# Performance work log

Hardware: AMD Instinct MI355X
Metric: run time of the kernel (lower is better)

The kernel has to match this reference:

```python
import jax, jax.numpy as jnp
import numpy as np

P, N, NF = 4, 871, 512            # num_meta_paths, node_size (hardcoded 871 in source), node_feature_size
XDIM = 116 * 116                   # x_proj input dim, hardcoded Linear(116*116, nf)
BETA, LAMBDA_WL, GAMMA = 0.1, 0.1, 0.1


def _xavier(k, shape):
    fan_in, fan_out = shape[0], shape[-1]
    bound = np.sqrt(6.0 / (fan_in + fan_out))
    return jax.random.uniform(k, shape, jnp.float32, -bound, bound)


def setup_inputs() -> dict:
    key = jax.random.key(0)
    ks = jax.random.split(key, 12)
    return {
        "z_stack": jax.random.normal(ks[0], (P, N, NF), jnp.float32),
        "x_orig": jax.random.normal(ks[1], (1, 116, 116), jnp.float32),
        "W": _xavier(ks[2], (N, 1)),
        "b": jax.random.uniform(ks[3], (N, 1), jnp.float32),
        "q": _xavier(ks[4], (N, NF)),
        "xp_w": _xavier(ks[5], (XDIM, NF)),
        "xp_b": jnp.zeros((NF,), jnp.float32),
        "w1": _xavier(ks[6], (2 * NF, 512)), "b1": jnp.zeros((512,), jnp.float32),
        "w2": _xavier(ks[7], (512, 256)), "b2": jnp.zeros((256,), jnp.float32),
        "w3": _xavier(ks[8], (256, 1)), "b3": jnp.zeros((1,), jnp.float32),
        "perm": jax.random.permutation(ks[9], N).astype(jnp.int32),
    }


def _mi_mlp(t, w1, b1, w2, b2, w3, b3):
    h = jax.nn.relu(t @ w1 + b1)
    h = jax.nn.relu(h @ w2 + b2)
    return h @ w3 + b3  # [N, 1]


def reference(z_stack, x_orig, W, b, q, xp_w, xp_b, w1, b1, w2, b2, w3, b3, perm):
    # --- vectorized form of the per-node loop:
    # score_p = mean_i( tanh(W_i * z[p,i,:] + b_i) . q_i )
    zt = jnp.tanh(W[None] * z_stack + b[None])            # [P,N,NF]
    scores = jnp.mean(jnp.sum(zt * q[None], axis=-1), axis=-1)  # [P]
    proportions = scores / jnp.sum(scores)
    attn = jax.nn.softmax(proportions)                    # [P] (no isomorphic pairs -> no overwrite)
    # layer_out_p = attn_p * z_p + z_p ; emb = sum_p layer_out_p
    emb = jnp.einsum('p,pnf->nf', 1.0 + attn, z_stack)    # [N,NF]
    # --- estimate_MI(x_orig, emb, mi_estimator_xz)
    x = jnp.broadcast_to(x_orig.reshape(1, -1), (N, XDIM))
    xh = x @ xp_w + xp_b                                  # [N,NF]
    t0 = jnp.concatenate([xh, emb], axis=1)               # [N,2NF]
    t1 = jnp.concatenate([xh, emb[perm]], axis=1)
    mi_lb = jnp.mean(_mi_mlp(t0, w1, b1, w2, b2, w3, b3)) - jnp.log(
        jnp.mean(jnp.exp(_mi_mlp(t1, w1, b1, w2, b2, w3, b3))) + 1e-8)
    I_XZ = jnp.clip(mi_lb, 0.0)
    # y_labels=None -> I_ZY = 0 ; empty isomorphic_pairs -> wl_loss = 0
    total_loss = I_XZ - BETA * 0.0 + LAMBDA_WL * 0.0 + GAMMA * jnp.sum(attn)
    return emb, total_loss
```

## Files before the change

### kernel.cpp

```cpp
#include <hip/hip_runtime.h>
#include <hip/hip_bf16.h>
#include <math.h>

#define NMETA  4
#define NNODE  871
#define NFEAT  512
#define XDIM   (116*116)
#define ZPLANE (NNODE*NFEAT)
#define MT     55

#define NXB    254
#define XROWS  53

#define WS_CNT    12
#define WS_SPART  16
#define WS_C1P    256
#define WS_XHP    2560
#define WS_V      132608
#define WS_W1P    133504
#define WS_W2P    264576

typedef short v8s __attribute__((ext_vector_type(8)));
typedef float v4f __attribute__((ext_vector_type(4)));

static __device__ __forceinline__ short f2bf(float f) {
  __hip_bfloat16 h = __float2bfloat16(f);
  return *reinterpret_cast<short*>(&h);
}

__global__ __launch_bounds__(1024) void k_front(const float* __restrict__ x,
                                                const float* __restrict__ xpw,
                                                const float* __restrict__ w1,
                                                const float* __restrict__ w2,
                                                const float* __restrict__ z,
                                                const float* __restrict__ W,
                                                const float* __restrict__ b,
                                                const float* __restrict__ q,
                                                float* __restrict__ ws,
                                                short* __restrict__ w1p,
                                                short* __restrict__ w2p) {
  const int blk = blockIdx.x;
  const int tid = threadIdx.x;

  if (blk < NXB) {
    const int d0 = blk * XROWS;
    const int rows = min(XROWS, XDIM - d0);
    __shared__ float xs[XROWS];
    __shared__ float4 redx[7][128];
    if (tid < rows) xs[tid] = x[d0 + tid];
    __syncthreads();
    const int f4 = tid & 127;
    const int g = tid >> 7;
    float4 acc = {0.f, 0.f, 0.f, 0.f};
    const float4* xp4 = (const float4*)xpw;
    for (int r = g; r < rows; r += 8) {
      const float xv = xs[r];
      const float4 wv = xp4[(size_t)(d0 + r) * 128 + f4];
      acc.x += xv * wv.x; acc.y += xv * wv.y; acc.z += xv * wv.z; acc.w += xv * wv.w;
    }
    if (g) redx[g - 1][f4] = acc;
    __syncthreads();
    if (!g) {
#pragma unroll
      for (int k = 0; k < 7; ++k) {
        float4 t = redx[k][f4];
        acc.x += t.x; acc.y += t.y; acc.z += t.z; acc.w += t.w;
      }
      ((float4*)(ws + WS_XHP + (size_t)blk * 512))[f4] = acc;
    }
  } else if (blk < NXB + MT) {
    const int sb = blk - NXB;
    const int row = tid >> 6;
    const int oc = tid & 63;
    const int gr = sb * 16 + row;
    const bool valid = gr < NNODE;
    const float4* z4 = (const float4*)z;
    const float4* q4 = (const float4*)q;
    float4 za0, za1, zb0, zb1, zc0, zc1, zd0, zd1, qa, qb;
    float wi = 0.f, bi = 0.f;
    za0 = za1 = zb0 = zb1 = zc0 = zc1 = zd0 = zd1 = (float4){0,0,0,0};
    qa = qb = (float4){0,0,0,0};
    const int zi = gr * 128 + oc * 2;
    if (valid) {
      za0 = z4[zi];                 za1 = z4[zi + 1];
      zb0 = z4[NNODE*128 + zi];     zb1 = z4[NNODE*128 + zi + 1];
      zc0 = z4[2*NNODE*128 + zi];   zc1 = z4[2*NNODE*128 + zi + 1];
      zd0 = z4[3*NNODE*128 + zi];   zd1 = z4[3*NNODE*128 + zi + 1];
      qa  = q4[zi];                 qb  = q4[zi + 1];
      wi = W[gr]; bi = b[gr];
    }
    auto dot8 = [&](const float4& u0, const float4& u1) -> float {
      return tanhf(wi*u0.x + bi)*qa.x + tanhf(wi*u0.y + bi)*qa.y
           + tanhf(wi*u0.z + bi)*qa.z + tanhf(wi*u0.w + bi)*qa.w
           + tanhf(wi*u1.x + bi)*qb.x + tanhf(wi*u1.y + bi)*qb.y
           + tanhf(wi*u1.z + bi)*qb.z + tanhf(wi*u1.w + bi)*qb.w;
    };
    float sp0 = valid ? dot8(za0, za1) : 0.f;
    float sp1 = valid ? dot8(zb0, zb1) : 0.f;
    float sp2 = valid ? dot8(zc0, zc1) : 0.f;
    float sp3 = valid ? dot8(zd0, zd1) : 0.f;
#pragma unroll
    for (int m = 1; m < 64; m <<= 1) {
      sp0 += __shfl_xor(sp0, m); sp1 += __shfl_xor(sp1, m);
      sp2 += __shfl_xor(sp2, m); sp3 += __shfl_xor(sp3, m);
    }
    __shared__ float sred[16][4];
    if (oc == 0) {
      sred[row][0] = sp0; sred[row][1] = sp1;
      sred[row][2] = sp2; sred[row][3] = sp3;
    }
    __syncthreads();
    if (tid < 4) {
      float s = 0.f;
#pragma unroll
      for (int r = 0; r < 16; ++r) s += sred[r][tid];
      ws[WS_SPART + tid * 55 + sb] = s;
    }
  } else {
    const int pb = blk - (NXB + MT);
    if (pb < 16) {
      const int s0 = pb * 16384;
#pragma unroll
      for (int it = 0; it < 16; ++it) {
        const int s = s0 + it * 1024 + tid;
        const int k = s >> 9, n = s & 511;
        const int t = (k >> 5) * 16384 + (n >> 4) * 512 + ((k >> 3) & 3) * 128
                    + (n & 15) * 8 + (k & 7);
        w1p[t] = f2bf(w1[(size_t)(512 + k) * 512 + n]);
      }
    } else {
      const int o0 = (pb - 16) * 16384;
#pragma unroll
      for (int it = 0; it < 16; ++it) {
        const int o = o0 + it * 1024 + tid;
        const int k = o >> 8, n = o & 255;
        const int t = (k >> 5) * 8192 + (n >> 4) * 512 + ((k >> 3) & 3) * 128
                    + (n & 15) * 8 + (k & 7);
        w2p[t] = f2bf(w2[(size_t)k * 256 + n]);
      }
    }
  }
}

__global__ __launch_bounds__(1024) void k_mid(const float* __restrict__ xpb,
                                              const float* __restrict__ w1,
                                              const float* __restrict__ b1,
                                              float* __restrict__ ws) {
  const int tid = threadIdx.x;
  if (blockIdx.x == 4) {
    if (tid == 0) *(unsigned*)&ws[WS_CNT] = 0u;
    return;
  }
  const int bk = blockIdx.x;
  __shared__ float xh[128];
  __shared__ float redr[1024];
  __shared__ float4 redg[7][128];
  const int f = tid & 127;
  const int part = tid >> 7;
  {
    float s = 0.f;
    for (int p = part; p < NXB; p += 8)
      s += ws[WS_XHP + (size_t)p * 512 + bk * 128 + f];
    redr[tid] = s;
  }
  __syncthreads();
  if (tid < 128) {
    float t = xpb[bk * 128 + tid];
#pragma unroll
    for (int g = 0; g < 8; ++g) t += redr[g * 128 + tid];
    xh[tid] = t;
  }
  __syncthreads();
  const int j4 = tid & 127;
  const int fg = tid >> 7;
  float4 acc = {0.f, 0.f, 0.f, 0.f};
  const float4* w14 = (const float4*)w1;
#pragma unroll
  for (int ff = 0; ff < 16; ++ff) {
    const int fr = bk * 128 + fg * 16 + ff;
    const float xv = xh[fg * 16 + ff];
    const float4 wv = w14[(size_t)fr * 128 + j4];
    acc.x += xv * wv.x; acc.y += xv * wv.y; acc.z += xv * wv.z; acc.w += xv * wv.w;
  }
  if (fg) redg[fg - 1][j4] = acc;
  __syncthreads();
  if (!fg) {
#pragma unroll
    for (int g = 0; g < 7; ++g) {
      float4 t = redg[g][j4];
      acc.x += t.x; acc.y += t.y; acc.z += t.z; acc.w += t.w;
    }
    if (bk == 0) {
      acc.x += b1[j4 * 4 + 0]; acc.y += b1[j4 * 4 + 1];
      acc.z += b1[j4 * 4 + 2]; acc.w += b1[j4 * 4 + 3];
    }
    ((float4*)(ws + WS_C1P + (size_t)bk * 512))[j4] = acc;
  }
}

__global__ __launch_bounds__(1024) void k_fused(const float* __restrict__ z,
                                                float* __restrict__ ws,
                                                float* __restrict__ out,
                                                const short* __restrict__ w1p,
                                                const short* __restrict__ w2p,
                                                const float* __restrict__ b2,
                                                const float* __restrict__ w3,
                                                const float* __restrict__ b3) {
  __shared__ __align__(16) short embs[8192];
  __shared__ __align__(16) short h2a[8192];
  __shared__ float cs[512];
  __shared__ float rf0[1024], rf1[1024];
  __shared__ float vred[16][17];
  __shared__ float cf[4];
  __shared__ float svred[4];
  const int tid = threadIdx.x;
  const int r0 = blockIdx.x * 16;
  const int oc = tid & 63;
  const int row = tid >> 6;
  const int gr = r0 + row;
  const bool valid = gr < NNODE;

  const float4* z4 = (const float4*)z;
  float4 za0, za1, zb0, zb1, zc0, zc1, zd0, zd1;
  za0 = za1 = zb0 = zb1 = zc0 = zc1 = zd0 = zd1 = (float4){0,0,0,0};
  const int zi = gr * 128 + oc * 2;
  if (valid) {
    za0 = z4[zi];                 za1 = z4[zi + 1];
    zb0 = z4[NNODE*128 + zi];     zb1 = z4[NNODE*128 + zi + 1];
    zc0 = z4[2*NNODE*128 + zi];   zc1 = z4[2*NNODE*128 + zi + 1];
    zd0 = z4[3*NNODE*128 + zi];   zd1 = z4[3*NNODE*128 + zi + 1];
  }

  if (tid < 512) {
    float a = 0.f;
#pragma unroll
    for (int k = 0; k < 4; ++k) a += ws[WS_C1P + k * 512 + tid];
    cs[tid] = a;
  }

  {
    const int w4 = tid >> 6;
    if (w4 < 4) {
      float v = (oc < 55) ? ws[WS_SPART + w4 * 55 + oc] : 0.f;
#pragma unroll
      for (int m = 1; m < 64; m <<= 1) v += __shfl_xor(v, m);
      if (oc == 0) svred[w4] = v;
    }
  }
  __syncthreads();
  if (tid == 0) {
    float sv[NMETA], sum = 0.f;
#pragma unroll
    for (int p = 0; p < NMETA; ++p) { sv[p] = svred[p] / (float)NNODE; sum += sv[p]; }
    float m = -1e30f;
#pragma unroll
    for (int p = 0; p < NMETA; ++p) { sv[p] = sv[p] / sum; m = fmaxf(m, sv[p]); }
    float es = 0.f;
#pragma unroll
    for (int p = 0; p < NMETA; ++p) { sv[p] = expf(sv[p] - m); es += sv[p]; }
#pragma unroll
    for (int p = 0; p < NMETA; ++p) cf[p] = 1.f + sv[p] / es;
  }
  __syncthreads();
  const float c0 = cf[0], c1c = cf[1], c2 = cf[2], c3 = cf[3];

  {
    const int slot = oc * 16 + (row ^ (oc & 15));
    v8s h;
    if (valid) {
      float4 r0v, r1v;
      r0v.x = c0*za0.x + c1c*zb0.x + c2*zc0.x + c3*zd0.x;
      r0v.y = c0*za0.y + c1c*zb0.y + c2*zc0.y + c3*zd0.y;
      r0v.z = c0*za0.z + c1c*zb0.z + c2*zc0.z + c3*zd0.z;
      r0v.w = c0*za0.w + c1c*zb0.w + c2*zc0.w + c3*zd0.w;
      r1v.x = c0*za1.x + c1c*zb1.x + c2*zc1.x + c3*zd1.x;
      r1v.y = c0*za1.y + c1c*zb1.y + c2*zc1.y + c3*zd1.y;
      r1v.z = c0*za1.z + c1c*zb1.z + c2*zc1.z + c3*zd1.z;
      r1v.w = c0*za1.w + c1c*zb1.w + c2*zc1.w + c3*zd1.w;
      ((float4*)out)[zi] = r0v;
      ((float4*)out)[zi + 1] = r1v;
      h[0] = f2bf(r0v.x); h[1] = f2bf(r0v.y); h[2] = f2bf(r0v.z); h[3] = f2bf(r0v.w);
      h[4] = f2bf(r1v.x); h[5] = f2bf(r1v.y); h[6] = f2bf(r1v.z); h[7] = f2bf(r1v.w);
    } else {
      h = (v8s){0,0,0,0,0,0,0,0};
    }
    *(v8s*)(embs + slot * 8) = h;
  }
  __syncthreads();

  const int lane = tid & 63, w = tid >> 6;
  const int n15 = lane & 15, quad = lane >> 4;
  v4f e[2];
#pragma unroll
  for (int ct = 0; ct < 2; ++ct) e[ct] = (v4f){0.f, 0.f, 0.f, 0.f};
#pragma unroll
  for (int kb = 0; kb < 16; ++kb) {
    const int koct = kb * 4 + quad;
    v8s a = *(const v8s*)(embs + (koct * 16 + (n15 ^ (koct & 15))) * 8);
    const short* B = w1p + kb * 16384 + w * 1024 + quad * 128 + n15 * 8;
#pragma unroll
    for (int ct = 0; ct < 2; ++ct) {
      v8s bb = *(const v8s*)(B + ct * 512);
      e[ct] = __builtin_amdgcn_mfma_f32_16x16x32_bf16(a, bb, e[ct], 0, 0, 0);
    }
  }
#pragma unroll
  for (int ct = 0; ct < 2; ++ct) {
    const int col = w * 32 + ct * 16 + n15;
    const int koct = col >> 3, j = col & 7;
#pragma unroll
    for (int r = 0; r < 4; ++r) {
      const int m = quad * 4 + r;
      h2a[(koct * 16 + (m ^ (koct & 15))) * 8 + j] = f2bf(fmaxf(e[ct][r] + cs[col], 0.f));
    }
  }
  __syncthreads();

  v4f g = (v4f){0.f, 0.f, 0.f, 0.f};
#pragma unroll
  for (int kb = 0; kb < 16; ++kb) {
    const int koct = kb * 4 + quad;
    v8s a = *(const v8s*)(h2a + (koct * 16 + (n15 ^ (koct & 15))) * 8);
    v8s bb = *(const v8s*)(w2p + kb * 8192 + w * 512 + quad * 128 + n15 * 8);
    g = __builtin_amdgcn_mfma_f32_16x16x32_bf16(a, bb, g, 0, 0, 0);
  }
  {
    const int col = w * 16 + n15;
    const float b2v = b2[col], w3v = w3[col];
#pragma unroll
    for (int r = 0; r < 4; ++r) {
      float s = fmaxf(g[r] + b2v, 0.f) * w3v;
      s += __shfl_xor(s, 1);
      s += __shfl_xor(s, 2);
      s += __shfl_xor(s, 4);
      s += __shfl_xor(s, 8);
      if (n15 == 0) vred[quad * 4 + r][w] = s;
    }
  }
  __syncthreads();
  if (tid < 16) {
    float acc = 0.f;
#pragma unroll
    for (int ww = 0; ww < 16; ++ww) acc += vred[tid][ww];
    const int grow = r0 + tid;
    if (grow < NNODE) ws[WS_V + grow] = acc;
  }

  __shared__ unsigned last;
  __syncthreads();
  if (tid == 0) {
    __threadfence();
    unsigned old = atomicAdd((unsigned int*)&ws[WS_CNT], 1u);
    last = (old == MT - 1) ? 1u : 0u;
  }
  __syncthreads();
  if (last) {
    __builtin_amdgcn_fence(__ATOMIC_ACQUIRE, "agent");
    const float bias = b3[0];
    float s0 = 0.f, s1 = 0.f;
    for (int i = tid; i < NNODE; i += 1024) {
      float xv = ws[WS_V + i] + bias;
      s0 += xv;
      s1 += expf(xv);
    }
    rf0[tid] = s0; rf1[tid] = s1;
    __syncthreads();
    for (int s = 512; s > 0; s >>= 1) {
      if (tid < s) { rf0[tid] += rf0[tid + s]; rf1[tid] += rf1[tid + s]; }
      __syncthreads();
    }
    if (tid == 0) {
      float m0 = rf0[0] / (float)NNODE;
      float m1 = rf1[0] / (float)NNODE;
      float mi = m0 - logf(m1 + 1e-8f);
      out[ZPLANE] = fmaxf(mi, 0.f) + 0.1f;
    }
  }
}

extern "C" void kernel_launch(void* const* d_in, const int* in_sizes, int n_in,
                              void* d_out, int out_size, void* d_ws, size_t ws_size,
                              hipStream_t stream) {
  const float* z   = (const float*)d_in[0];
  const float* x   = (const float*)d_in[1];
  const float* W   = (const float*)d_in[2];
  const float* b   = (const float*)d_in[3];
  const float* q   = (const float*)d_in[4];
  const float* xpw = (const float*)d_in[5];
  const float* xpb = (const float*)d_in[6];
  const float* w1  = (const float*)d_in[7];
  const float* b1  = (const float*)d_in[8];
  const float* w2  = (const float*)d_in[9];
  const float* b2  = (const float*)d_in[10];
  const float* w3  = (const float*)d_in[11];
  const float* b3  = (const float*)d_in[12];
  float* out = (float*)d_out;
  float* ws  = (float*)d_ws;

  short* w1p = (short*)(ws + WS_W1P);
  short* w2p = (short*)(ws + WS_W2P);

  k_front<<<NXB + MT + 20, 1024, 0, stream>>>(x, xpw, w1, w2, z, W, b, q,
                                              ws, w1p, w2p);
  k_mid<<<5, 1024, 0, stream>>>(xpb, w1, b1, ws);
  k_fused<<<MT, 1024, 0, stream>>>(z, ws, out, w1p, w2p, b2, w3, b3);
}
```

Measured before the change: 139.9 us.

## Use output buffer as scratch and replace last-block reduction with atomics plus grid spin barrier

Scratch data (partial sums, packed bf16 weights, counters) now lives inside the output buffer instead of the workspace, and the emb output is written only after all blocks reach a spin barrier, so the scratch regions are overwritten last. The final MI reduction now uses per-block float atomics into two accumulators rather than a last-block pass over per-row values, and k_mid loses its counter-reset block. The grid-wide spin wait assumes all 55 blocks are co-resident, and float atomics make the summation order nondeterministic.

Result: no change. 140.4 us (+0.4%).

```diff
diff --git a/kernel.cpp b/kernel.cpp
--- a/kernel.cpp
+++ b/kernel.cpp
@@ -12,13 +12,14 @@
 #define NXB    254
 #define XROWS  53
 
-#define WS_CNT    12
-#define WS_SPART  16
-#define WS_C1P    256
-#define WS_XHP    2560
-#define WS_V      132608
-#define WS_W1P    133504
-#define WS_W2P    264576
+#define SC_S0     0
+#define SC_S1     1
+#define SC_CNT    2
+#define SC_SPART  16
+#define SC_C1P    256
+#define SC_XHP    2560
+#define SC_W1P    140000
+#define SC_W2P    280000
 
 typedef short v8s __attribute__((ext_vector_type(8)));
 typedef float v4f __attribute__((ext_vector_type(4)));
@@ -36,11 +37,11 @@
                                                 const float* __restrict__ W,
                                                 const float* __restrict__ b,
                                                 const float* __restrict__ q,
-                                                float* __restrict__ ws,
-                                                short* __restrict__ w1p,
-                                                short* __restrict__ w2p) {
+                                                float* __restrict__ out) {
   const int blk = blockIdx.x;
   const int tid = threadIdx.x;
+  short* w1p = (short*)(out + SC_W1P);
+  short* w2p = (short*)(out + SC_W2P);
 
   if (blk < NXB) {
     const int d0 = blk * XROWS;
@@ -66,7 +67,7 @@
         float4 t = redx[k][f4];
         acc.x += t.x; acc.y += t.y; acc.z += t.z; acc.w += t.w;
       }
-      ((float4*)(ws + WS_XHP + (size_t)blk * 512))[f4] = acc;
+      ((float4*)(out + SC_XHP + (size_t)blk * 512))[f4] = acc;
     }
   } else if (blk < NXB + MT) {
     const int sb = blk - NXB;
@@ -114,10 +115,15 @@
       float s = 0.f;
 #pragma unroll
       for (int r = 0; r < 16; ++r) s += sred[r][tid];
-      ws[WS_SPART + tid * 55 + sb] = s;
+      out[SC_SPART + tid * 55 + sb] = s;
     }
   } else {
     const int pb = blk - (NXB + MT);
+    if (pb == 0 && tid == 0) {
+      out[SC_S0] = 0.f;
+      out[SC_S1] = 0.f;
+      *(unsigned*)&out[SC_CNT] = 0u;
+    }
     if (pb < 16) {
       const int s0 = pb * 16384;
 #pragma unroll
@@ -145,12 +151,8 @@
 __global__ __launch_bounds__(1024) void k_mid(const float* __restrict__ xpb,
                                               const float* __restrict__ w1,
                                               const float* __restrict__ b1,
-                                              float* __restrict__ ws) {
+                                              float* __restrict__ out) {
   const int tid = threadIdx.x;
-  if (blockIdx.x == 4) {
-    if (tid == 0) *(unsigned*)&ws[WS_CNT] = 0u;
-    return;
-  }
   const int bk = blockIdx.x;
   __shared__ float xh[128];
   __shared__ float redr[1024];
@@ -160,7 +162,7 @@
   {
     float s = 0.f;
     for (int p = part; p < NXB; p += 8)
-      s += ws[WS_XHP + (size_t)p * 512 + bk * 128 + f];
+      s += out[SC_XHP + (size_t)p * 512 + bk * 128 + f];
     redr[tid] = s;
   }
   __syncthreads();
@@ -194,12 +196,11 @@
       acc.x += b1[j4 * 4 + 0]; acc.y += b1[j4 * 4 + 1];
       acc.z += b1[j4 * 4 + 2]; acc.w += b1[j4 * 4 + 3];
     }
-    ((float4*)(ws + WS_C1P + (size_t)bk * 512))[j4] = acc;
+    ((float4*)(out + SC_C1P + (size_t)bk * 512))[j4] = acc;
   }
 }
 
 __global__ __launch_bounds__(1024) void k_fused(const float* __restrict__ z,
-                                                float* __restrict__ ws,
                                                 float* __restrict__ out,
                                                 const short* __restrict__ w1p,
                                                 const short* __restrict__ w2p,
@@ -209,7 +210,6 @@
   __shared__ __align__(16) short embs[8192];
   __shared__ __align__(16) short h2a[8192];
   __shared__ float cs[512];
-  __shared__ float rf0[1024], rf1[1024];
   __shared__ float vred[16][17];
   __shared__ float cf[4];
   __shared__ float svred[4];
@@ -234,14 +234,14 @@
   if (tid < 512) {
     float a = 0.f;
 #pragma unroll
-    for (int k = 0; k < 4; ++k) a += ws[WS_C1P + k * 512 + tid];
+    for (int k = 0; k < 4; ++k) a += out[SC_C1P + k * 512 + tid];
     cs[tid] = a;
   }
 
   {
     const int w4 = tid >> 6;
     if (w4 < 4) {
-      float v = (oc < 55) ? ws[WS_SPART + w4 * 55 + oc] : 0.f;
+      float v = (oc < 55) ? out[SC_SPART + w4 * 55 + oc] : 0.f;
 #pragma unroll
       for (int m = 1; m < 64; m <<= 1) v += __shfl_xor(v, m);
       if (oc == 0) svred[w4] = v;
@@ -264,11 +264,11 @@
   __syncthreads();
   const float c0 = cf[0], c1c = cf[1], c2 = cf[2], c3 = cf[3];
 
+  float4 r0v = {0,0,0,0}, r1v = {0,0,0,0};
   {
     const int slot = oc * 16 + (row ^ (oc & 15));
     v8s h;
     if (valid) {
-      float4 r0v, r1v;
       r0v.x = c0*za0.x + c1c*zb0.x + c2*zc0.x + c3*zd0.x;
       r0v.y = c0*za0.y + c1c*zb0.y + c2*zc0.y + c3*zd0.y;
       r0v.z = c0*za0.z + c1c*zb0.z + c2*zc0.z + c3*zd0.z;
@@ -277,8 +277,6 @@
       r1v.y = c0*za1.y + c1c*zb1.y + c2*zc1.y + c3*zd1.y;
       r1v.z = c0*za1.z + c1c*zb1.z + c2*zc1.z + c3*zd1.z;
       r1v.w = c0*za1.w + c1c*zb1.w + c2*zc1.w + c3*zd1.w;
-      ((float4*)out)[zi] = r0v;
-      ((float4*)out)[zi + 1] = r1v;
       h[0] = f2bf(r0v.x); h[1] = f2bf(r0v.y); h[2] = f2bf(r0v.z); h[3] = f2bf(r0v.w);
       h[4] = f2bf(r1v.x); h[5] = f2bf(r1v.y); h[6] = f2bf(r1v.z); h[7] = f2bf(r1v.w);
     } else {
@@ -338,43 +336,47 @@
     }
   }
   __syncthreads();
+
   if (tid < 16) {
     float acc = 0.f;
 #pragma unroll
     for (int ww = 0; ww < 16; ++ww) acc += vred[tid][ww];
-    const int grow = r0 + tid;
-    if (grow < NNODE) ws[WS_V + grow] = acc;
-  }
-
-  __shared__ unsigned last;
-  __syncthreads();
+    const bool vrow = (r0 + tid) < NNODE;
+    const float xv = acc + b3[0];
+    float s0p = vrow ? xv : 0.f;
+    float s1p = vrow ? expf(xv) : 0.f;
+    s0p += __shfl_xor(s0p, 1); s1p += __shfl_xor(s1p, 1);
+    s0p += __shfl_xor(s0p, 2); s1p += __shfl_xor(s1p, 2);
+    s0p += __shfl_xor(s0p, 4); s1p += __shfl_xor(s1p, 4);
+    s0p += __shfl_xor(s0p, 8); s1p += __shfl_xor(s1p, 8);
+    if (tid == 0) {
+      atomicAdd(&out[SC_S0], s0p);
+      atomicAdd(&out[SC_S1], s1p);
+      __hip_atomic_fetch_add((unsigned*)&out[SC_CNT], 1u,
+                             __ATOMIC_RELEASE, __HIP_MEMORY_SCOPE_AGENT);
+    }
+  }
+
   if (tid == 0) {
-    __threadfence();
-    unsigned old = atomicAdd((unsigned int*)&ws[WS_CNT], 1u);
-    last = (old == MT - 1) ? 1u : 0u;
-  }
-  __syncthreads();
-  if (last) {
-    __builtin_amdgcn_fence(__ATOMIC_ACQUIRE, "agent");
-    const float bias = b3[0];
-    float s0 = 0.f, s1 = 0.f;
-    for (int i = tid; i < NNODE; i += 1024) {
-      float xv = ws[WS_V + i] + bias;
-      s0 += xv;
-      s1 += expf(xv);
-    }
-    rf0[tid] = s0; rf1[tid] = s1;
-    __syncthreads();
-    for (int s = 512; s > 0; s >>= 1) {
-      if (tid < s) { rf0[tid] += rf0[tid + s]; rf1[tid] += rf1[tid + s]; }
-      __syncthreads();
-    }
-    if (tid == 0) {
-      float m0 = rf0[0] / (float)NNODE;
-      float m1 = rf1[0] / (float)NNODE;
-      float mi = m0 - logf(m1 + 1e-8f);
-      out[ZPLANE] = fmaxf(mi, 0.f) + 0.1f;
-    }
+    while (__hip_atomic_load((const unsigned*)&out[SC_CNT], __ATOMIC_RELAXED,
+                             __HIP_MEMORY_SCOPE_AGENT) != (unsigned)MT)
+      __builtin_amdgcn_s_sleep(2);
+  }
+  __syncthreads();
+
+  if (valid) {
+    ((float4*)out)[zi] = r0v;
+    ((float4*)out)[zi + 1] = r1v;
+  }
+  if (blockIdx.x == 0 && tid == 0) {
+    float t0 = __hip_atomic_load(&out[SC_S0], __ATOMIC_RELAXED,
+                                 __HIP_MEMORY_SCOPE_AGENT);
+    float t1 = __hip_atomic_load(&out[SC_S1], __ATOMIC_RELAXED,
+                                 __HIP_MEMORY_SCOPE_AGENT);
+    float m0 = t0 / (float)NNODE;
+    float m1 = t1 / (float)NNODE;
+    float mi = m0 - logf(m1 + 1e-8f);
+    out[ZPLANE] = fmaxf(mi, 0.f) + 0.1f;
   }
 }
 
@@ -395,13 +397,12 @@
   const float* w3  = (const float*)d_in[11];
   const float* b3  = (const float*)d_in[12];
   float* out = (float*)d_out;
-  float* ws  = (float*)d_ws;
-
-  short* w1p = (short*)(ws + WS_W1P);
-  short* w2p = (short*)(ws + WS_W2P);
-
-  k_front<<<NXB + MT + 20, 1024, 0, stream>>>(x, xpw, w1, w2, z, W, b, q,
-                                              ws, w1p, w2p);
-  k_mid<<<5, 1024, 0, stream>>>(xpb, w1, b1, ws);
-  k_fused<<<MT, 1024, 0, stream>>>(z, ws, out, w1p, w2p, b2, w3, b3);
+  (void)d_ws; (void)ws_size;
+
+  const short* w1p = (const short*)(out + SC_W1P);
+  const short* w2p = (const short*)(out + SC_W2P);
+
+  k_front<<<NXB + MT + 20, 1024, 0, stream>>>(x, xpw, w1, w2, z, W, b, q, out);
+  k_mid<<<4, 1024, 0, stream>>>(xpb, w1, b1, out);
+  k_fused<<<MT, 1024, 0, stream>>>(z, out, w1p, w2p, b2, w3, b3);
 }
```
